# Performance work log

Hardware: AMD Instinct MI355X
Metric: run time of the kernel (lower is better)

The kernel has to match this reference:

```python
import jax, jax.numpy as jnp
import numpy as np

B, S, D_IN, D_MODEL = 8, 2048, 512, 512
NEG_INF = -1e9  # matches masked_fill value -1000000000.0


def setup_inputs() -> dict:
    key = jax.random.key(0)
    ks = jax.random.split(key, 7)
    scale = 1.0 / np.sqrt(D_IN).astype(np.float32)
    return {
        "x": jax.random.normal(ks[0], (B, S, D_IN), dtype=jnp.float32),
        "pad_mask": jnp.zeros((B, S), dtype=bool),
        "Wq": jax.random.normal(ks[1], (D_MODEL, D_IN), dtype=jnp.float32) * scale,
        "bq": jax.random.normal(ks[2], (D_MODEL,), dtype=jnp.float32) * 0.01,
        "Wk": jax.random.normal(ks[3], (D_MODEL, D_IN), dtype=jnp.float32) * scale,
        "bk": jax.random.normal(ks[4], (D_MODEL,), dtype=jnp.float32) * 0.01,
        "Wv": jax.random.normal(ks[5], (D_MODEL, D_IN), dtype=jnp.float32) * scale,
        "bv": jax.random.normal(ks[6], (D_MODEL,), dtype=jnp.float32) * 0.01,
    }


def reference(x, pad_mask, Wq, bq, Wk, bk, Wv, bv):
    # Linear projections (torch Linear: y = x @ W.T + b)
    q = jnp.einsum('bsd,md->bsm', x, Wq) + bq  # [B,S,M]
    k = jnp.einsum('bsd,md->bsm', x, Wk) + bk
    v = jnp.einsum('bsd,md->bsm', x, Wv) + bv
    inv_sqrt_m = jnp.float32(1.0 / np.sqrt(D_MODEL))
    s = jnp.einsum('bqm,bkm->bqk', q, k) * inv_sqrt_m  # [B,S,S]
    # pad mask broadcasts over query dim (pad_mask.unsqueeze(1) in torch)
    s = jnp.where(pad_mask[:, None, :], NEG_INF, s)
    # masked (causal) attention: upper triangle above diagonal is blocked
    causal = jnp.triu(jnp.ones((S, S), dtype=bool), k=1)
    s = jnp.where(causal[None, :, :], NEG_INF, s)
    scores = jax.nn.softmax(s, axis=-1)
    # dropout p=0.0 / eval mode -> identity
    return jnp.einsum('bqk,bkm->bqm', scores, v)
```

## Files before the change

### kernel.cpp

```cpp
#include <hip/hip_runtime.h>
#include <hip/hip_bf16.h>


typedef __attribute__((ext_vector_type(8))) short short8;
typedef __attribute__((ext_vector_type(4))) float f32x4;

#define S_    2048
#define DM    512
#define SCALE 0.04419417382415922f

static __device__ __forceinline__ unsigned short f2bf(float f) {
    __hip_bfloat16 h = __float2bfloat16(f);
    unsigned short u;
    __builtin_memcpy(&u, &h, sizeof(u));
    return u;
}
static __device__ __forceinline__ float bf2f(unsigned short u) {
    union { unsigned int i; float f; } c;
    c.i = ((unsigned int)u) << 16;
    return c.f;
}

static __device__ __forceinline__ void gload16(const void* g, void* l) {
    __builtin_amdgcn_global_load_lds(
        (const __attribute__((address_space(1))) void*)g,
        (__attribute__((address_space(3))) void*)l, 16, 0, 0);
}

static __device__ __forceinline__ void stage_tile(
    const unsigned short* __restrict__ gbase, size_t ld,
    unsigned short (*lds)[64], int w, int lane)
{
    const int srow = lane >> 3;
    const int scol = (lane & 7) * 8;
    #pragma unroll
    for (int t = 0; t < 4; t++) {
        const int row = w * 32 + t * 8 + srow;
        gload16(gbase + (size_t)row * ld + scol, &lds[w * 32 + t * 8][0]);
    }
}

static __device__ __forceinline__ void stage32(
    const unsigned short* __restrict__ gbase, size_t ld,
    unsigned short (*lds)[32], int w, int lane)
{
    const int srow = lane >> 2;
    const int scol = (lane & 3) * 8;
    #pragma unroll
    for (int t = 0; t < 2; t++) {
        const int row = w * 32 + t * 16 + srow;
        gload16(gbase + (size_t)row * ld + scol, &lds[w * 32 + t * 16][0]);
    }
}

static __device__ __forceinline__ void mfma_step(
    const unsigned short (*Ash)[64], const unsigned short (*Bsh)[64],
    f32x4 acc[4][4], int wm, int wn, int lr, int lg)
{
    #pragma unroll
    for (int kk = 0; kk < 2; kk++) {
        short8 af[4], bf[4];
        #pragma unroll
        for (int m = 0; m < 4; m++)
            af[m] = *reinterpret_cast<const short8*>(&Ash[wm * 64 + m * 16 + lr][kk * 32 + lg * 8]);
        #pragma unroll
        for (int n = 0; n < 4; n++)
            bf[n] = *reinterpret_cast<const short8*>(&Bsh[wn * 64 + n * 16 + lr][kk * 32 + lg * 8]);
        #pragma unroll
        for (int m = 0; m < 4; m++)
            #pragma unroll
            for (int n = 0; n < 4; n++)
                acc[m][n] = __builtin_amdgcn_mfma_f32_16x16x32_bf16(af[m], bf[n], acc[m][n], 0, 0, 0);
    }
}

__global__ __launch_bounds__(256) void cvt_all(
    const float* __restrict__ x,
    const float* __restrict__ wq, const float* __restrict__ wk, const float* __restrict__ wv,
    unsigned short* __restrict__ xb,
    unsigned short* __restrict__ wqb, unsigned short* __restrict__ wkb,
    unsigned short* __restrict__ wvb)
{
    const int bid = blockIdx.x;
    const float* src; unsigned short* dst; int i;
    if (bid < 8192) { src = x; dst = xb; i = bid * 256 + threadIdx.x; }
    else {
        const int r = bid - 8192;
        const int m = r >> 8;
        src = (m == 0) ? wq : (m == 1) ? wk : wv;
        dst = (m == 0) ? wqb : (m == 1) ? wkb : wvb;
        i = (r & 255) * 256 + threadIdx.x;
    }
    float4 v = reinterpret_cast<const float4*>(src)[i];
    ushort4 o;
    o.x = f2bf(v.x); o.y = f2bf(v.y); o.z = f2bf(v.z); o.w = f2bf(v.w);
    reinterpret_cast<ushort4*>(dst)[i] = o;
}

__global__ __launch_bounds__(256) void qk_proj(
    const unsigned short* __restrict__ X,
    const unsigned short* __restrict__ Wqb, const unsigned short* __restrict__ Wkb,
    const float* __restrict__ bq, const float* __restrict__ bk,
    unsigned short* __restrict__ Dq, unsigned short* __restrict__ Dk)
{
    __shared__ unsigned short smem[2][3][128][32];

    const int m0 = blockIdx.x * 128;
    const int n0 = blockIdx.y * 128;

    const int tid  = threadIdx.x;
    const int lane = tid & 63;
    const int w    = tid >> 6;
    const int wm   = w >> 1, wn = w & 1;
    const int lr   = lane & 15, lg = lane >> 4;

    f32x4 accq[4][4], acck[4][4];
    #pragma unroll
    for (int m = 0; m < 4; m++)
        #pragma unroll
        for (int n = 0; n < 4; n++) {
            accq[m][n] = (f32x4){0.f, 0.f, 0.f, 0.f};
            acck[m][n] = (f32x4){0.f, 0.f, 0.f, 0.f};
        }

    stage32(&X[(size_t)m0 * DM], DM, smem[0][0], w, lane);
    stage32(&Wqb[(size_t)n0 * DM], DM, smem[0][1], w, lane);
    stage32(&Wkb[(size_t)n0 * DM], DM, smem[0][2], w, lane);
    __syncthreads();
    int cur = 0;
    for (int t = 0; t < 16; t++) {
        if (t < 15) {
            const int k0 = (t + 1) * 32;
            stage32(&X[(size_t)m0 * DM + k0], DM, smem[cur ^ 1][0], w, lane);
            stage32(&Wqb[(size_t)n0 * DM + k0], DM, smem[cur ^ 1][1], w, lane);
            stage32(&Wkb[(size_t)n0 * DM + k0], DM, smem[cur ^ 1][2], w, lane);
        }
        short8 af[4], bqf[4], bkf[4];
        #pragma unroll
        for (int m = 0; m < 4; m++)
            af[m] = *reinterpret_cast<const short8*>(&smem[cur][0][wm * 64 + m * 16 + lr][lg * 8]);
        #pragma unroll
        for (int n = 0; n < 4; n++) {
            bqf[n] = *reinterpret_cast<const short8*>(&smem[cur][1][wn * 64 + n * 16 + lr][lg * 8]);
            bkf[n] = *reinterpret_cast<const short8*>(&smem[cur][2][wn * 64 + n * 16 + lr][lg * 8]);
        }
        #pragma unroll
        for (int m = 0; m < 4; m++)
            #pragma unroll
            for (int n = 0; n < 4; n++) {
                accq[m][n] = __builtin_amdgcn_mfma_f32_16x16x32_bf16(af[m], bqf[n], accq[m][n], 0, 0, 0);
                acck[m][n] = __builtin_amdgcn_mfma_f32_16x16x32_bf16(af[m], bkf[n], acck[m][n], 0, 0, 0);
            }
        __syncthreads();
        cur ^= 1;
    }

    unsigned short (*Csh)[128] = reinterpret_cast<unsigned short (*)[128]>(&smem[0][0][0][0]);
    #pragma unroll
    for (int n = 0; n < 4; n++) {
        int ct = wn * 64 + n * 16 + lr;
        float bcol = bq[n0 + ct];
        #pragma unroll
        for (int m = 0; m < 4; m++) {
            int rt = wm * 64 + m * 16 + lg * 4;
            #pragma unroll
            for (int j = 0; j < 4; j++) {
                int row = rt + j;
                Csh[row][ct ^ ((row & 7) << 3)] = f2bf(accq[m][n][j] + bcol);
            }
        }
    }
    __syncthreads();
    #pragma unroll
    for (int i = 0; i < 8; i++) {
        int chunk = i * 256 + tid;
        int row = chunk >> 4, cb = (chunk & 15) * 8;
        short8 vv = *reinterpret_cast<const short8*>(&Csh[row][cb ^ ((row & 7) << 3)]);
        *reinterpret_cast<short8*>(&Dq[(size_t)(m0 + row) * DM + n0 + cb]) = vv;
    }
    __syncthreads();
    #pragma unroll
    for (int n = 0; n < 4; n++) {
        int ct = wn * 64 + n * 16 + lr;
        float bcol = bk[n0 + ct];
        #pragma unroll
        for (int m = 0; m < 4; m++) {
            int rt = wm * 64 + m * 16 + lg * 4;
            #pragma unroll
            for (int j = 0; j < 4; j++) {
                int row = rt + j;
                Csh[row][ct ^ ((row & 7) << 3)] = f2bf(acck[m][n][j] + bcol);
            }
        }
    }
    __syncthreads();
    #pragma unroll
    for (int i = 0; i < 8; i++) {
        int chunk = i * 256 + tid;
        int row = chunk >> 4, cb = (chunk & 15) * 8;
        short8 vv = *reinterpret_cast<const short8*>(&Csh[row][cb ^ ((row & 7) << 3)]);
        *reinterpret_cast<short8*>(&Dk[(size_t)(m0 + row) * DM + n0 + cb]) = vv;
    }
}

__global__ __launch_bounds__(256) void vt_gemm(
    const unsigned short* __restrict__ X, const unsigned short* __restrict__ Wvb,
    const float* __restrict__ bv, unsigned short* __restrict__ Dvt)
{
    __shared__ unsigned short smem[2][2][128][64];

    const int m0 = blockIdx.y * 128;
    const int n0 = blockIdx.x * 128;

    const int tid  = threadIdx.x;
    const int lane = tid & 63;
    const int w    = tid >> 6;
    const int wm   = w >> 1, wn = w & 1;
    const int lr   = lane & 15, lg = lane >> 4;

    f32x4 acc[4][4];
    #pragma unroll
    for (int m = 0; m < 4; m++)
        #pragma unroll
        for (int n = 0; n < 4; n++) acc[m][n] = (f32x4){0.f, 0.f, 0.f, 0.f};

    stage_tile(&Wvb[(size_t)m0 * DM], DM, smem[0][0], w, lane);
    stage_tile(&X[(size_t)n0 * DM], DM, smem[0][1], w, lane);
    __syncthreads();
    int cur = 0;
    for (int t = 0; t < 8; t++) {
        if (t < 7) {
            const int k0 = (t + 1) * 64;
            stage_tile(&Wvb[(size_t)m0 * DM + k0], DM, smem[cur ^ 1][0], w, lane);
            stage_tile(&X[(size_t)n0 * DM + k0], DM, smem[cur ^ 1][1], w, lane);
        }
        mfma_step(smem[cur][0], smem[cur][1], acc, wm, wn, lr, lg);
        __syncthreads();
        cur ^= 1;
    }

    unsigned short (*Csh)[128] = reinterpret_cast<unsigned short (*)[128]>(&smem[0][0][0][0]);
    #pragma unroll
    for (int n = 0; n < 4; n++) {
        int ct = wn * 64 + n * 16 + lr;
        #pragma unroll
        for (int m = 0; m < 4; m++) {
            int rt = wm * 64 + m * 16 + lg * 4;
            #pragma unroll
            for (int j = 0; j < 4; j++) {
                int row = rt + j;
                Csh[row][ct ^ ((row & 7) << 3)] = f2bf(acc[m][n][j] + bv[m0 + row]);
            }
        }
    }
    __syncthreads();
    #pragma unroll
    for (int i = 0; i < 8; i++) {
        int chunk = i * 256 + tid;
        int row = chunk >> 4, cb = (chunk & 15) * 8;
        short8 vv = *reinterpret_cast<const short8*>(&Csh[row][cb ^ ((row & 7) << 3)]);
        *reinterpret_cast<short8*>(&Dvt[(size_t)(m0 + row) * 16384 + n0 + cb]) = vv;
    }
}

__global__ __launch_bounds__(256) void qk_gemm(
    const unsigned short* __restrict__ Qg, const unsigned short* __restrict__ Kg,
    const unsigned char* __restrict__ pad, unsigned short* __restrict__ Sp,
    float* __restrict__ partial)
{
    __shared__ unsigned short smem[2][2][128][64];

    const int wgid = blockIdx.x;
    const int b = wgid & 7;
    const int l = wgid >> 3;
    int it = (int)((sqrtf(8.f * l + 1.f) - 1.f) * 0.5f);
    while ((it + 1) * (it + 2) / 2 <= l) ++it;
    while (it * (it + 1) / 2 > l) --it;
    const int jt = l - it * (it + 1) / 2;

    const unsigned short* __restrict__ A = Qg + (size_t)b * S_ * DM;
    const unsigned short* __restrict__ B = Kg + (size_t)b * S_ * DM;
    unsigned short* __restrict__ Sw = Sp + ((size_t)b * 136 + l) * 16384;
    const int m0 = it * 128, n0 = jt * 128;

    const int tid  = threadIdx.x;
    const int lane = tid & 63;
    const int w    = tid >> 6;
    const int wm   = w >> 1, wn = w & 1;
    const int lr   = lane & 15, lg = lane >> 4;

    f32x4 acc[4][4];
    #pragma unroll
    for (int m = 0; m < 4; m++)
        #pragma unroll
        for (int n = 0; n < 4; n++) acc[m][n] = (f32x4){0.f, 0.f, 0.f, 0.f};

    stage_tile(&A[(size_t)m0 * DM], DM, smem[0][0], w, lane);
    stage_tile(&B[(size_t)n0 * DM], DM, smem[0][1], w, lane);
    __syncthreads();
    int cur = 0;
    for (int t = 0; t < 8; t++) {
        if (t < 7) {
            const int k0 = (t + 1) * 64;
            stage_tile(&A[(size_t)m0 * DM + k0], DM, smem[cur ^ 1][0], w, lane);
            stage_tile(&B[(size_t)n0 * DM + k0], DM, smem[cur ^ 1][1], w, lane);
        }
        mfma_step(smem[cur][0], smem[cur][1], acc, wm, wn, lr, lg);
        __syncthreads();
        cur ^= 1;
    }

    unsigned short (*Csh)[128] = reinterpret_cast<unsigned short (*)[128]>(&smem[0][0][0][0]);
    #pragma unroll
    for (int n = 0; n < 4; n++) {
        int ct = wn * 64 + n * 16 + lr;
        int colg = n0 + ct;
        bool pd = pad[(size_t)b * S_ + colg] != 0;
        #pragma unroll
        for (int m = 0; m < 4; m++) {
            int rt = wm * 64 + m * 16 + lg * 4;
            #pragma unroll
            for (int j = 0; j < 4; j++) {
                int row = rt + j;
                float p = (pd || colg > m0 + row) ? 0.f : __expf(acc[m][n][j] * SCALE);
                Csh[row][ct ^ ((row & 7) << 3)] = f2bf(p);
            }
        }
    }
    __syncthreads();
    #pragma unroll
    for (int i = 0; i < 8; i++) {
        int chunk = i * 256 + tid;
        int row = chunk >> 4, cb = (chunk & 15) * 8;
        short8 vv = *reinterpret_cast<const short8*>(&Csh[row][cb ^ ((row & 7) << 3)]);
        *reinterpret_cast<short8*>(&Sw[(size_t)row * 128 + cb]) = vv;
        float s = 0.f;
        #pragma unroll
        for (int e = 0; e < 8; e++) s += bf2f((unsigned short)vv[e]);
        #pragma unroll
        for (int msk = 1; msk < 16; msk <<= 1) s += __shfl_xor(s, msk);
        if ((lane & 15) == 0)
            partial[((size_t)b * S_ + m0 + row) * 16 + jt] = s;
    }
}

__global__ __launch_bounds__(256) void pv_gemm(
    const unsigned short* __restrict__ Sp, const unsigned short* __restrict__ VT,
    const float* __restrict__ partial, float* __restrict__ Out)
{
    __shared__ unsigned short smem[2][2][128][64];

    const int wgid = blockIdx.x;
    const int b  = wgid & 7;
    const int r  = wgid >> 3;
    const int it = (r < 32) ? (15 - (r >> 2)) : ((r >> 2) - 8);
    const int nb = r & 3;
    const int m0 = it * 128, n0 = nb * 128;
    const int nt = (it + 1) * 2;
    const unsigned short* __restrict__ Abase =
        Sp + ((size_t)b * 136 + (size_t)it * (it + 1) / 2) * 16384;

    const int tid  = threadIdx.x;
    const int lane = tid & 63;
    const int w    = tid >> 6;
    const int wm   = w >> 1, wn = w & 1;
    const int lr   = lane & 15, lg = lane >> 4;

    f32x4 acc[4][4];
    #pragma unroll
    for (int m = 0; m < 4; m++)
        #pragma unroll
        for (int n = 0; n < 4; n++) acc[m][n] = (f32x4){0.f, 0.f, 0.f, 0.f};

    stage_tile(Abase, 128, smem[0][0], w, lane);
    stage_tile(&VT[(size_t)n0 * 16384 + (size_t)b * S_], 16384, smem[0][1], w, lane);
    __syncthreads();
    int cur = 0;
    for (int t = 0; t < nt; t++) {
        if (t + 1 < nt) {
            const int k0 = (t + 1) * 64;
            stage_tile(Abase + (size_t)(k0 >> 7) * 16384 + (k0 & 127), 128, smem[cur ^ 1][0], w, lane);
            stage_tile(&VT[(size_t)n0 * 16384 + (size_t)b * S_ + k0], 16384, smem[cur ^ 1][1], w, lane);
        }
        mfma_step(smem[cur][0], smem[cur][1], acc, wm, wn, lr, lg);
        __syncthreads();
        cur ^= 1;
    }

    float* Lsh = reinterpret_cast<float*>(&smem[0][0][0][0]);
    if (tid < 128) {
        const float* pr = &partial[((size_t)b * S_ + m0 + tid) * 16];
        float s = 0.f;
        for (int j = 0; j <= it; j++) s += pr[j];
        Lsh[tid] = 1.f / s;
    }
    __syncthreads();

    #pragma unroll
    for (int n = 0; n < 4; n++) {
        int col = n0 + wn * 64 + n * 16 + lr;
        #pragma unroll
        for (int m = 0; m < 4; m++) {
            int rowb = wm * 64 + m * 16 + lg * 4;
            #pragma unroll
            for (int j = 0; j < 4; j++) {
                int row = rowb + j;
                float li = Lsh[row];
                Out[((size_t)(b * S_ + m0 + row)) * DM + col] = acc[m][n][j] * li;
            }
        }
    }
}

extern "C" void kernel_launch(void* const* d_in, const int* in_sizes, int n_in,
                              void* d_out, int out_size, void* d_ws, size_t ws_size,
                              hipStream_t stream) {
    const float* x  = (const float*)d_in[0];
    const unsigned char* pad = (const unsigned char*)d_in[1];
    const float* Wq = (const float*)d_in[2];
    const float* bq = (const float*)d_in[3];
    const float* Wk = (const float*)d_in[4];
    const float* bk = (const float*)d_in[5];
    const float* Wv = (const float*)d_in[6];
    const float* bv = (const float*)d_in[7];
    float* out = (float*)d_out;

    char* ws = (char*)d_ws;
    unsigned short* vtb     = (unsigned short*)(ws);
    float*          partial = (float*)(ws + 16777216);
    unsigned short* Spacked = (unsigned short*)(ws + 17825792);
    unsigned short* xb      = (unsigned short*)(ws + 17825792);
    unsigned short* wqb     = (unsigned short*)(ws + 53477376);
    unsigned short* wkb     = wqb + 262144;
    unsigned short* wvb     = wqb + 524288;

    unsigned short* qb = (unsigned short*)d_out;
    unsigned short* kb = qb + 8388608;

    cvt_all<<<8960, 256, 0, stream>>>(x, Wq, Wk, Wv, xb, wqb, wkb, wvb);

    dim3 gp2(128, 4);
    qk_proj<<<gp2, 256, 0, stream>>>(xb, wqb, wkb, bq, bk, qb, kb);

    dim3 gv(128, 4);
    vt_gemm<<<gv, 256, 0, stream>>>(xb, wvb, bv, vtb);

    qk_gemm<<<1088, 256, 0, stream>>>(qb, kb, pad, Spacked, partial);

    pv_gemm<<<512, 256, 0, stream>>>(Spacked, vtb, partial, out);
}
```

Before: 126.4 us.

## Widen QK score tiles to 128x256 with K-step 32 triple buffers

The QK^T kernel now computes 128x256 tiles instead of 128x128. Each Q tile is reused across twice as many key columns, and the workgroup count nearly halves (576 vs 1088). Staging switches to 32-wide K slices with three LDS buffers (A plus two B halves), and each wave runs 4x8 MFMAs per step. The packed score layout, the partial-sum indexing and the PV kernel's addressing are adjusted to match. The trade-off is more accumulator registers, which may lower occupancy, and some wasted work on diagonal tiles where half of a 256-wide tile can be fully masked.

After: 136.6 us. +8.1%, slower.

```diff
diff --git a/kernel.cpp b/kernel.cpp
--- a/kernel.cpp
+++ b/kernel.cpp
@@ -268,20 +268,20 @@
     const unsigned char* __restrict__ pad, unsigned short* __restrict__ Sp,
     float* __restrict__ partial)
 {
-    __shared__ unsigned short smem[2][2][128][64];
+    __shared__ unsigned short lds[32768];
+    unsigned short (*stg)[3][128][32] = reinterpret_cast<unsigned short (*)[3][128][32]>(lds);
 
     const int wgid = blockIdx.x;
     const int b = wgid & 7;
-    const int l = wgid >> 3;
-    int it = (int)((sqrtf(8.f * l + 1.f) - 1.f) * 0.5f);
-    while ((it + 1) * (it + 2) / 2 <= l) ++it;
-    while (it * (it + 1) / 2 > l) --it;
-    const int jt = l - it * (it + 1) / 2;
+    const int p = wgid >> 3;
+    int it = 0;
+    while (((it + 1) * (it + 3) + ((it + 1) & 1)) / 4 <= p) ++it;
+    const int jp = p - (it * (it + 2) + (it & 1)) / 4;
+    const int m0 = it * 128, n0 = jp * 256;
 
     const unsigned short* __restrict__ A = Qg + (size_t)b * S_ * DM;
     const unsigned short* __restrict__ B = Kg + (size_t)b * S_ * DM;
-    unsigned short* __restrict__ Sw = Sp + ((size_t)b * 136 + l) * 16384;
-    const int m0 = it * 128, n0 = jt * 128;
+    unsigned short* __restrict__ Sw = Sp + ((size_t)b * 72 + p) * 32768;
 
     const int tid  = threadIdx.x;
     const int lane = tid & 63;
@@ -289,31 +289,44 @@
     const int wm   = w >> 1, wn = w & 1;
     const int lr   = lane & 15, lg = lane >> 4;
 
-    f32x4 acc[4][4];
+    f32x4 acc[4][8];
     #pragma unroll
     for (int m = 0; m < 4; m++)
         #pragma unroll
-        for (int n = 0; n < 4; n++) acc[m][n] = (f32x4){0.f, 0.f, 0.f, 0.f};
-
-    stage_tile(&A[(size_t)m0 * DM], DM, smem[0][0], w, lane);
-    stage_tile(&B[(size_t)n0 * DM], DM, smem[0][1], w, lane);
+        for (int n = 0; n < 8; n++) acc[m][n] = (f32x4){0.f, 0.f, 0.f, 0.f};
+
+    stage32(&A[(size_t)m0 * DM], DM, stg[0][0], w, lane);
+    stage32(&B[(size_t)n0 * DM], DM, stg[0][1], w, lane);
+    stage32(&B[(size_t)(n0 + 128) * DM], DM, stg[0][2], w, lane);
     __syncthreads();
     int cur = 0;
-    for (int t = 0; t < 8; t++) {
-        if (t < 7) {
-            const int k0 = (t + 1) * 64;
-            stage_tile(&A[(size_t)m0 * DM + k0], DM, smem[cur ^ 1][0], w, lane);
-            stage_tile(&B[(size_t)n0 * DM + k0], DM, smem[cur ^ 1][1], w, lane);
-        }
-        mfma_step(smem[cur][0], smem[cur][1], acc, wm, wn, lr, lg);
+    for (int t = 0; t < 16; t++) {
+        if (t < 15) {
+            const int k0 = (t + 1) * 32;
+            stage32(&A[(size_t)m0 * DM + k0], DM, stg[cur ^ 1][0], w, lane);
+            stage32(&B[(size_t)n0 * DM + k0], DM, stg[cur ^ 1][1], w, lane);
+            stage32(&B[(size_t)(n0 + 128) * DM + k0], DM, stg[cur ^ 1][2], w, lane);
+        }
+        short8 af[4], bf[8];
+        #pragma unroll
+        for (int m = 0; m < 4; m++)
+            af[m] = *reinterpret_cast<const short8*>(&stg[cur][0][wm * 64 + m * 16 + lr][lg * 8]);
+        #pragma unroll
+        for (int n = 0; n < 8; n++)
+            bf[n] = *reinterpret_cast<const short8*>(&stg[cur][1 + wn][n * 16 + lr][lg * 8]);
+        #pragma unroll
+        for (int m = 0; m < 4; m++)
+            #pragma unroll
+            for (int n = 0; n < 8; n++)
+                acc[m][n] = __builtin_amdgcn_mfma_f32_16x16x32_bf16(af[m], bf[n], acc[m][n], 0, 0, 0);
         __syncthreads();
         cur ^= 1;
     }
 
-    unsigned short (*Csh)[128] = reinterpret_cast<unsigned short (*)[128]>(&smem[0][0][0][0]);
-    #pragma unroll
-    for (int n = 0; n < 4; n++) {
-        int ct = wn * 64 + n * 16 + lr;
+    unsigned short (*Csh)[256] = reinterpret_cast<unsigned short (*)[256]>(lds);
+    #pragma unroll
+    for (int n = 0; n < 8; n++) {
+        int ct = wn * 128 + n * 16 + lr;
         int colg = n0 + ct;
         bool pd = pad[(size_t)b * S_ + colg] != 0;
         #pragma unroll
@@ -322,25 +335,25 @@
             #pragma unroll
             for (int j = 0; j < 4; j++) {
                 int row = rt + j;
-                float p = (pd || colg > m0 + row) ? 0.f : __expf(acc[m][n][j] * SCALE);
-                Csh[row][ct ^ ((row & 7) << 3)] = f2bf(p);
-            }
-        }
-    }
-    __syncthreads();
-    #pragma unroll
-    for (int i = 0; i < 8; i++) {
+                float pv = (pd || colg > m0 + row) ? 0.f : __expf(acc[m][n][j] * SCALE);
+                Csh[row][ct ^ ((row & 7) << 3)] = f2bf(pv);
+            }
+        }
+    }
+    __syncthreads();
+    #pragma unroll
+    for (int i = 0; i < 16; i++) {
         int chunk = i * 256 + tid;
-        int row = chunk >> 4, cb = (chunk & 15) * 8;
+        int row = chunk >> 5, cb = (chunk & 31) * 8;
         short8 vv = *reinterpret_cast<const short8*>(&Csh[row][cb ^ ((row & 7) << 3)]);
-        *reinterpret_cast<short8*>(&Sw[(size_t)row * 128 + cb]) = vv;
+        *reinterpret_cast<short8*>(&Sw[(size_t)row * 256 + cb]) = vv;
         float s = 0.f;
         #pragma unroll
         for (int e = 0; e < 8; e++) s += bf2f((unsigned short)vv[e]);
         #pragma unroll
-        for (int msk = 1; msk < 16; msk <<= 1) s += __shfl_xor(s, msk);
-        if ((lane & 15) == 0)
-            partial[((size_t)b * S_ + m0 + row) * 16 + jt] = s;
+        for (int msk = 1; msk < 32; msk <<= 1) s += __shfl_xor(s, msk);
+        if ((lane & 31) == 0)
+            partial[((size_t)b * S_ + m0 + row) * 8 + jp] = s;
     }
 }
 
@@ -358,7 +371,7 @@
     const int m0 = it * 128, n0 = nb * 128;
     const int nt = (it + 1) * 2;
     const unsigned short* __restrict__ Abase =
-        Sp + ((size_t)b * 136 + (size_t)it * (it + 1) / 2) * 16384;
+        Sp + ((size_t)b * 72 + (it * (it + 2) + (it & 1)) / 4) * 32768;
 
     const int tid  = threadIdx.x;
     const int lane = tid & 63;
@@ -372,14 +385,14 @@
         #pragma unroll
         for (int n = 0; n < 4; n++) acc[m][n] = (f32x4){0.f, 0.f, 0.f, 0.f};
 
-    stage_tile(Abase, 128, smem[0][0], w, lane);
+    stage_tile(Abase, 256, smem[0][0], w, lane);
     stage_tile(&VT[(size_t)n0 * 16384 + (size_t)b * S_], 16384, smem[0][1], w, lane);
     __syncthreads();
     int cur = 0;
     for (int t = 0; t < nt; t++) {
         if (t + 1 < nt) {
             const int k0 = (t + 1) * 64;
-            stage_tile(Abase + (size_t)(k0 >> 7) * 16384 + (k0 & 127), 128, smem[cur ^ 1][0], w, lane);
+            stage_tile(Abase + (size_t)(k0 >> 8) * 32768 + (k0 & 255), 256, smem[cur ^ 1][0], w, lane);
             stage_tile(&VT[(size_t)n0 * 16384 + (size_t)b * S_ + k0], 16384, smem[cur ^ 1][1], w, lane);
         }
         mfma_step(smem[cur][0], smem[cur][1], acc, wm, wn, lr, lg);
@@ -389,9 +402,9 @@
 
     float* Lsh = reinterpret_cast<float*>(&smem[0][0][0][0]);
     if (tid < 128) {
-        const float* pr = &partial[((size_t)b * S_ + m0 + tid) * 16];
+        const float* pr = &partial[((size_t)b * S_ + m0 + tid) * 8];
         float s = 0.f;
-        for (int j = 0; j <= it; j++) s += pr[j];
+        for (int j = 0; j <= (it >> 1); j++) s += pr[j];
         Lsh[tid] = 1.f / s;
     }
     __syncthreads();
@@ -428,9 +441,9 @@
     char* ws = (char*)d_ws;
     unsigned short* vtb     = (unsigned short*)(ws);
     float*          partial = (float*)(ws + 16777216);
-    unsigned short* Spacked = (unsigned short*)(ws + 17825792);
-    unsigned short* xb      = (unsigned short*)(ws + 17825792);
-    unsigned short* wqb     = (unsigned short*)(ws + 53477376);
+    unsigned short* Spacked = (unsigned short*)(ws + 17301504);
+    unsigned short* xb      = (unsigned short*)(ws + 17301504);
+    unsigned short* wqb     = (unsigned short*)(ws + 55050240);
     unsigned short* wkb     = wqb + 262144;
     unsigned short* wvb     = wqb + 524288;
 
@@ -445,7 +458,7 @@
     dim3 gv(128, 4);
     vt_gemm<<<gv, 256, 0, stream>>>(xb, wvb, bv, vtb);
 
-    qk_gemm<<<1088, 256, 0, stream>>>(qb, kb, pad, Spacked, partial);
+    qk_gemm<<<576, 256, 0, stream>>>(qb, kb, pad, Spacked, partial);
 
     pv_gemm<<<512, 256, 0, stream>>>(Spacked, vtb, partial, out);
 }
```

## Deepen QK and PV GEMM pipelines with prefetch two tiles ahead

Applied to the files above, without the earlier changes.

Restructures the QK^T and PV GEMM main loops so global-to-LDS loads are issued two k-steps ahead. Each step reads all fragments into registers first, then refills the same buffer while the MFMAs run. Explicit vmcnt and lgkmcnt waits, s_barrier and sched_barrier replace __syncthreads to control overlap. The aim is to hide global load latency behind MFMA work, at the cost of more fragment registers and fragile hand-written wait counts.

Result: slower. 130.2 us (+3.0%).

```diff
diff --git a/kernel.cpp b/kernel.cpp
--- a/kernel.cpp
+++ b/kernel.cpp
@@ -51,6 +51,33 @@
         const int row = w * 32 + t * 16 + srow;
         gload16(gbase + (size_t)row * ld + scol, &lds[w * 32 + t * 16][0]);
     }
+}
+
+static __device__ __forceinline__ void read_frags(
+    const unsigned short (*Ash)[64], const unsigned short (*Bsh)[64],
+    short8 (&af)[2][4], short8 (&bf)[2][4], int wm, int wn, int lr, int lg)
+{
+    #pragma unroll
+    for (int kk = 0; kk < 2; kk++) {
+        #pragma unroll
+        for (int m = 0; m < 4; m++)
+            af[kk][m] = *reinterpret_cast<const short8*>(&Ash[wm * 64 + m * 16 + lr][kk * 32 + lg * 8]);
+        #pragma unroll
+        for (int n = 0; n < 4; n++)
+            bf[kk][n] = *reinterpret_cast<const short8*>(&Bsh[wn * 64 + n * 16 + lr][kk * 32 + lg * 8]);
+    }
+}
+
+static __device__ __forceinline__ void mfma_all(
+    const short8 (&af)[2][4], const short8 (&bf)[2][4], f32x4 (&acc)[4][4])
+{
+    #pragma unroll
+    for (int kk = 0; kk < 2; kk++)
+        #pragma unroll
+        for (int m = 0; m < 4; m++)
+            #pragma unroll
+            for (int n = 0; n < 4; n++)
+                acc[m][n] = __builtin_amdgcn_mfma_f32_16x16x32_bf16(af[kk][m], bf[kk][n], acc[m][n], 0, 0, 0);
 }
 
 static __device__ __forceinline__ void mfma_step(
@@ -297,18 +324,43 @@
 
     stage_tile(&A[(size_t)m0 * DM], DM, smem[0][0], w, lane);
     stage_tile(&B[(size_t)n0 * DM], DM, smem[0][1], w, lane);
-    __syncthreads();
+    stage_tile(&A[(size_t)m0 * DM + 64], DM, smem[1][0], w, lane);
+    stage_tile(&B[(size_t)n0 * DM + 64], DM, smem[1][1], w, lane);
+    asm volatile("s_waitcnt vmcnt(8)" ::: "memory");
+    __builtin_amdgcn_s_barrier();
+    __builtin_amdgcn_sched_barrier(0);
+
     int cur = 0;
-    for (int t = 0; t < 8; t++) {
-        if (t < 7) {
-            const int k0 = (t + 1) * 64;
-            stage_tile(&A[(size_t)m0 * DM + k0], DM, smem[cur ^ 1][0], w, lane);
-            stage_tile(&B[(size_t)n0 * DM + k0], DM, smem[cur ^ 1][1], w, lane);
-        }
-        mfma_step(smem[cur][0], smem[cur][1], acc, wm, wn, lr, lg);
-        __syncthreads();
+    for (int t = 0; t < 6; t++) {
+        short8 af[2][4], bf[2][4];
+        read_frags(smem[cur][0], smem[cur][1], af, bf, wm, wn, lr, lg);
+        asm volatile("s_waitcnt lgkmcnt(0)" ::: "memory");
+        __builtin_amdgcn_sched_barrier(0);
+        __builtin_amdgcn_s_barrier();
+        __builtin_amdgcn_sched_barrier(0);
+        const int k0 = (t + 2) * 64;
+        stage_tile(&A[(size_t)m0 * DM + k0], DM, smem[cur][0], w, lane);
+        stage_tile(&B[(size_t)n0 * DM + k0], DM, smem[cur][1], w, lane);
+        mfma_all(af, bf, acc);
+        __builtin_amdgcn_sched_barrier(0);
+        asm volatile("s_waitcnt vmcnt(8)" ::: "memory");
+        __builtin_amdgcn_s_barrier();
+        __builtin_amdgcn_sched_barrier(0);
         cur ^= 1;
     }
+    {
+        short8 af[2][4], bf[2][4];
+        read_frags(smem[cur][0], smem[cur][1], af, bf, wm, wn, lr, lg);
+        mfma_all(af, bf, acc);
+        __builtin_amdgcn_sched_barrier(0);
+        asm volatile("s_waitcnt vmcnt(0)" ::: "memory");
+        __builtin_amdgcn_s_barrier();
+        __builtin_amdgcn_sched_barrier(0);
+        cur ^= 1;
+        read_frags(smem[cur][0], smem[cur][1], af, bf, wm, wn, lr, lg);
+        mfma_all(af, bf, acc);
+    }
+    __syncthreads();
 
     unsigned short (*Csh)[128] = reinterpret_cast<unsigned short (*)[128]>(&smem[0][0][0][0]);
     #pragma unroll
@@ -359,6 +411,7 @@
     const int nt = (it + 1) * 2;
     const unsigned short* __restrict__ Abase =
         Sp + ((size_t)b * 136 + (size_t)it * (it + 1) / 2) * 16384;
+    const size_t vtoff = (size_t)n0 * 16384 + (size_t)b * S_;
 
     const int tid  = threadIdx.x;
     const int lane = tid & 63;
@@ -373,19 +426,44 @@
         for (int n = 0; n < 4; n++) acc[m][n] = (f32x4){0.f, 0.f, 0.f, 0.f};
 
     stage_tile(Abase, 128, smem[0][0], w, lane);
-    stage_tile(&VT[(size_t)n0 * 16384 + (size_t)b * S_], 16384, smem[0][1], w, lane);
-    __syncthreads();
+    stage_tile(&VT[vtoff], 16384, smem[0][1], w, lane);
+    stage_tile(Abase + 64, 128, smem[1][0], w, lane);
+    stage_tile(&VT[vtoff + 64], 16384, smem[1][1], w, lane);
+    asm volatile("s_waitcnt vmcnt(8)" ::: "memory");
+    __builtin_amdgcn_s_barrier();
+    __builtin_amdgcn_sched_barrier(0);
+
     int cur = 0;
-    for (int t = 0; t < nt; t++) {
-        if (t + 1 < nt) {
-            const int k0 = (t + 1) * 64;
-            stage_tile(Abase + (size_t)(k0 >> 7) * 16384 + (k0 & 127), 128, smem[cur ^ 1][0], w, lane);
-            stage_tile(&VT[(size_t)n0 * 16384 + (size_t)b * S_ + k0], 16384, smem[cur ^ 1][1], w, lane);
-        }
-        mfma_step(smem[cur][0], smem[cur][1], acc, wm, wn, lr, lg);
-        __syncthreads();
+    for (int t = 0; t < nt - 2; t++) {
+        short8 af[2][4], bf[2][4];
+        read_frags(smem[cur][0], smem[cur][1], af, bf, wm, wn, lr, lg);
+        asm volatile("s_waitcnt lgkmcnt(0)" ::: "memory");
+        __builtin_amdgcn_sched_barrier(0);
+        __builtin_amdgcn_s_barrier();
+        __builtin_amdgcn_sched_barrier(0);
+        const int k0 = (t + 2) * 64;
+        stage_tile(Abase + (size_t)(k0 >> 7) * 16384 + (k0 & 127), 128, smem[cur][0], w, lane);
+        stage_tile(&VT[vtoff + k0], 16384, smem[cur][1], w, lane);
+        mfma_all(af, bf, acc);
+        __builtin_amdgcn_sched_barrier(0);
+        asm volatile("s_waitcnt vmcnt(8)" ::: "memory");
+        __builtin_amdgcn_s_barrier();
+        __builtin_amdgcn_sched_barrier(0);
         cur ^= 1;
     }
+    {
+        short8 af[2][4], bf[2][4];
+        read_frags(smem[cur][0], smem[cur][1], af, bf, wm, wn, lr, lg);
+        mfma_all(af, bf, acc);
+        __builtin_amdgcn_sched_barrier(0);
+        asm volatile("s_waitcnt vmcnt(0)" ::: "memory");
+        __builtin_amdgcn_s_barrier();
+        __builtin_amdgcn_sched_barrier(0);
+        cur ^= 1;
+        read_frags(smem[cur][0], smem[cur][1], af, bf, wm, wn, lr, lg);
+        mfma_all(af, bf, acc);
+    }
+    __syncthreads();
 
     float* Lsh = reinterpret_cast<float*>(&smem[0][0][0][0]);
     if (tid < 128) {
```
